# Performance work log

Hardware: AMD Instinct MI355X
Metric: run time of the kernel (lower is better)

Reference implementation:

```python
import jax, jax.numpy as jnp
import numpy as np

N_NODES = 50000
N_EDGES = 800000
F_IN = 128
HID = 32
H_IN = 4
N_CLS = 47
H_OUT = 4
NEG_SLOPE = 0.2


def _param(k, shape, scale=0.1):
    return jax.random.normal(k, shape, dtype=jnp.float32) * scale


def setup_inputs() -> dict:
    key = jax.random.key(0)
    ks = jax.random.split(key, 14)
    return {
        "x": jax.random.normal(ks[0], (N_NODES, F_IN), dtype=jnp.float32),
        "edge_index": jax.random.randint(ks[1], (2, N_EDGES), 0, N_NODES, dtype=jnp.int64),
        # layer 1: in -> hidden, heads_in, concat
        "W1": _param(ks[2], (F_IN, H_IN * HID)),
        "a1s": _param(ks[3], (H_IN, HID)),
        "a1d": _param(ks[4], (H_IN, HID)),
        "b1": _param(ks[5], (H_IN * HID,)),
        # layer 2: hidden*heads -> hidden, heads_in, concat
        "W2": _param(ks[6], (H_IN * HID, H_IN * HID)),
        "a2s": _param(ks[7], (H_IN, HID)),
        "a2d": _param(ks[8], (H_IN, HID)),
        "b2": _param(ks[9], (H_IN * HID,)),
        # layer 3: hidden*heads -> out, heads_out, mean (concat=False)
        "W3": _param(ks[10], (H_IN * HID, H_OUT * N_CLS)),
        "a3s": _param(ks[11], (H_OUT, N_CLS)),
        "a3d": _param(ks[12], (H_OUT, N_CLS)),
        "b3": _param(ks[13], (N_CLS,)),
    }


def gat_conv(x, W, att_src, att_dst, bias, src, dst, concat):
    """PyG GATConv (self-loops pre-appended in src/dst, eval mode)."""
    n = x.shape[0]
    H, C = att_src.shape
    h = (x @ W).reshape(n, H, C)                      # [N, H, C]
    a_src = jnp.sum(h * att_src[None], axis=-1)       # [N, H]
    a_dst = jnp.sum(h * att_dst[None], axis=-1)       # [N, H]
    alpha = a_src[src] + a_dst[dst]                   # [E, H]
    alpha = jnp.where(alpha >= 0, alpha, NEG_SLOPE * alpha)
    # segment softmax over destination nodes
    m = jax.ops.segment_max(alpha, dst, num_segments=n)  # [N, H]
    e = jnp.exp(alpha - m[dst])
    denom = jax.ops.segment_sum(e, dst, num_segments=n)  # [N, H]
    w = e / denom[dst]                                   # [E, H]
    msg = h[src] * w[:, :, None]                         # [E, H, C]
    out = jax.ops.segment_sum(msg, dst, num_segments=n)  # [N, H, C]
    if concat:
        out = out.reshape(n, H * C)
    else:
        out = out.mean(axis=1)
    return out + bias


def reference(x, edge_index, W1, a1s, a1d, b1, W2, a2s, a2d, b2, W3, a3s, a3d, b3):
    n = x.shape[0]
    loops = jnp.arange(n, dtype=edge_index.dtype)
    src = jnp.concatenate([edge_index[0], loops])
    dst = jnp.concatenate([edge_index[1], loops])
    h = gat_conv(x, W1, a1s, a1d, b1, src, dst, concat=True)
    h = jax.nn.relu(h)
    h = gat_conv(h, W2, a2s, a2d, b2, src, dst, concat=True)
    h = jax.nn.relu(h)
    h = gat_conv(h, W3, a3s, a3d, b3, src, dst, concat=False)
    return jax.nn.log_softmax(h, axis=1)
```

## Files before the change

kernel.cpp:

```cpp
#include <hip/hip_runtime.h>

typedef unsigned short u16;
typedef unsigned int uint32;
typedef __attribute__((ext_vector_type(8))) short short8;
typedef __attribute__((ext_vector_type(4))) float float4v;

#define N_NODES 50000
#define N_EDGES 800000
#define N_TOT   850000
#define NBH 256
#define NB_BKT ((N_NODES + 255) >> 8)
#define NODE_BLOCKS ((N_NODES + 3) / 4)

__device__ __forceinline__ float b2f(u16 u) {
  return __uint_as_float(((unsigned int)u) << 16);
}
__device__ __forceinline__ u16 f2b(float f) {
  unsigned int x = __float_as_uint(f);
  unsigned int r = (x + 0x7fffu + ((x >> 16) & 1u)) >> 16;
  return (u16)r;
}
__device__ __forceinline__ float lo_bf(uint32 g) { return __uint_as_float(g << 16); }
__device__ __forceinline__ float hi_bf(uint32 g) { return __uint_as_float(g & 0xffff0000u); }
__device__ __forceinline__ u16 conv_elem(const void* src, int i, int isf32) {
  if (isf32) return f2b(((const float*)src)[i]);
  return ((const u16*)src)[i];
}
__device__ __forceinline__ float lrelu(float a) { return (a >= 0.f) ? a : 0.2f * a; }
__device__ __forceinline__ int eget(const int* __restrict__ ei, int i, int isI64) {
  return isI64 ? ei[2 * i] : ei[i];
}

__global__ void detect_mode(const u16* __restrict__ x16, const int* __restrict__ ei32,
                            int* __restrict__ flags) {
  __shared__ int sh_f32, sh_i32;
  int tid = threadIdx.x;
  if (tid == 0) { sh_f32 = 0; sh_i32 = 0; }
  __syncthreads();
  int emax = 0;
  for (int i = tid; i < 4096; i += 256) {
    int e = (x16[i] >> 7) & 0xFF;
    emax = emax > e ? emax : e;
  }
  if (emax >= 140) atomicOr(&sh_f32, 1);
  if (ei32[2 * tid + 1] != 0) atomicOr(&sh_i32, 1);
  __syncthreads();
  if (tid == 0) { flags[0] = sh_f32; flags[1] = sh_i32 ? 0 : 1; }
}

__global__ void reorder_all(const void* W1, const void* W2, const void* W3,
                            const void* a1s, const void* a1d, const void* b1,
                            const void* a2s, const void* a2d, const void* b2,
                            const void* a3s, const void* a3d, const void* b3,
                            const int* __restrict__ flags,
                            u16* __restrict__ Wf1, u16* __restrict__ Wf2,
                            u16* __restrict__ Wf3, u16* __restrict__ wt) {
  int idx = blockIdx.x * blockDim.x + threadIdx.x;
  int f32 = flags[0];
  if (idx < 57344) {
    const void* W; u16* Wf; int NCOLS, li;
    if (idx < 16384)      { W = W1; Wf = Wf1; NCOLS = 128; li = idx; }
    else if (idx < 32768) { W = W2; Wf = Wf2; NCOLS = 128; li = idx - 16384; }
    else                  { W = W3; Wf = Wf3; NCOLS = 188; li = idx - 32768; }
    int j = li & 7;
    int l = (li >> 3) & 63;
    int c = (li >> 9) & 3;
    int t = li >> 11;
    int k = c * 32 + (l >> 4) * 8 + j;
    int n = t * 16 + (l & 15);
    Wf[li] = (n < NCOLS) ? conv_elem(W, k * NCOLS + n, f32) : (u16)0;
  } else {
    int li = idx - 57344;
    const void* src; int off;
    if (li < 128)       { src = a1s; off = 16384; }
    else if (li < 256)  { src = a1d; off = 16512; li -= 128; }
    else if (li < 384)  { src = b1;  off = 16640; li -= 256; }
    else if (li < 512)  { src = a2s; off = 33152; li -= 384; }
    else if (li < 640)  { src = a2d; off = 33280; li -= 512; }
    else if (li < 768)  { src = b2;  off = 33408; li -= 640; }
    else if (li < 956)  { src = a3s; off = 57600; li -= 768; }
    else if (li < 1144) { src = a3d; off = 57788; li -= 956; }
    else if (li < 1191) { src = b3;  off = 57976; li -= 1144; }
    else return;
    wt[off + li] = conv_elem(src, li, f32);
  }
}


__global__ __launch_bounds__(256) void pack_hist(const int* __restrict__ ei,
                                                 const int* __restrict__ flags,
                                                 uint32* __restrict__ epack,
                                                 int* __restrict__ cnt, int nE) {
  __shared__ int hist[NB_BKT];
  for (int t = threadIdx.x; t < NB_BKT; t += 256) hist[t] = 0;
  __syncthreads();
  const int i64 = flags[1];
  const int chunk = (nE + NBH - 1) / NBH;
  const int lo = blockIdx.x * chunk;
  const int hi = min(lo + chunk, nE);
  for (int e = lo + (int)threadIdx.x; e < hi; e += 256) {
    int s = eget(ei, e, i64);
    int d = eget(ei, nE + e, i64);
    epack[e] = ((uint32)d << 16) | (uint32)s;
    atomicAdd(&hist[d >> 8], 1);
  }
  __syncthreads();
  for (int t = threadIdx.x; t < NB_BKT; t += 256) cnt[t * NBH + blockIdx.x] = hist[t];
}

__global__ __launch_bounds__(256) void scan_cols(int* __restrict__ cnt,
                                                 int* __restrict__ total) {
  __shared__ int ws[4];
  const int bkt = blockIdx.x;
  const int tid = threadIdx.x, lane = tid & 63, wv = tid >> 6;
  int v = cnt[bkt * NBH + tid];
  int incl = v;
#pragma unroll
  for (int off = 1; off < 64; off <<= 1) {
    int t = __shfl_up(incl, off, 64);
    if (lane >= off) incl += t;
  }
  if (lane == 63) ws[wv] = incl;
  __syncthreads();
  if (tid == 0) {
    int s = 0;
#pragma unroll
    for (int w = 0; w < 4; w++) { int t = ws[w]; ws[w] = s; s += t; }
    total[bkt] = s;
  }
  __syncthreads();
  cnt[bkt * NBH + tid] = ws[wv] + incl - v;
}

__global__ __launch_bounds__(256) void scan_base(const int* __restrict__ total,
                                                 int* __restrict__ base) {
  __shared__ int ws[4];
  const int tid = threadIdx.x, lane = tid & 63, wv = tid >> 6;
  int v = (tid < NB_BKT) ? total[tid] : 0;
  int incl = v;
#pragma unroll
  for (int off = 1; off < 64; off <<= 1) {
    int t = __shfl_up(incl, off, 64);
    if (lane >= off) incl += t;
  }
  if (lane == 63) ws[wv] = incl;
  __syncthreads();
  if (tid == 0) {
    int s = 0;
#pragma unroll
    for (int w = 0; w < 4; w++) { int t = ws[w]; ws[w] = s; s += t; }
    base[NB_BKT] = s;
  }
  __syncthreads();
  if (tid < NB_BKT) base[tid] = ws[wv] + incl - v;
}

__global__ __launch_bounds__(256) void scatter_coarse(const uint32* __restrict__ epack,
                                                      const int* __restrict__ cnt,
                                                      const int* __restrict__ base,
                                                      uint32* __restrict__ staging, int nE) {
  __shared__ int lcur[NB_BKT];
  for (int t = threadIdx.x; t < NB_BKT; t += 256)
    lcur[t] = base[t] + cnt[t * NBH + blockIdx.x];
  __syncthreads();
  const int chunk = (nE + NBH - 1) / NBH;
  const int lo = blockIdx.x * chunk;
  const int hi = min(lo + chunk, nE);
  for (int e = lo + (int)threadIdx.x; e < hi; e += 256) {
    uint32 pk = epack[e];
    int p = atomicAdd(&lcur[pk >> 24], 1);
    staging[p] = pk;
  }
}

__global__ __launch_bounds__(256) void build_csr(const uint32* __restrict__ staging,
                                                 const int* __restrict__ base,
                                                 int* __restrict__ row_start,
                                                 int* __restrict__ csr_src32, int nN) {
  __shared__ int hist[256];
  __shared__ int cur[256];
  __shared__ int ws[4];
  const int b = blockIdx.x;
  const int tid = threadIdx.x;
  const int lane = tid & 63, wv = tid >> 6;
  hist[tid] = 0;
  __syncthreads();
  const int lo = base[b], hi = base[b + 1];
  for (int i = lo + tid; i < hi; i += 256)
    atomicAdd(&hist[(staging[i] >> 16) & 255], 1);
  __syncthreads();
  int v = hist[tid];
  int incl = v;
#pragma unroll
  for (int off = 1; off < 64; off <<= 1) {
    int t = __shfl_up(incl, off, 64);
    if (lane >= off) incl += t;
  }
  if (lane == 63) ws[wv] = incl;
  __syncthreads();
  if (tid == 0) {
    int s = 0;
#pragma unroll
    for (int w = 0; w < 4; w++) { int t = ws[w]; ws[w] = s; s += t; }
  }
  __syncthreads();
  int excl = ws[wv] + incl - v;
  const int n = (b << 8) + tid;
  if (n < nN) {
    int rs = lo + (b << 8) + excl + tid;
    row_start[n] = rs;
    csr_src32[rs] = n;
    cur[tid] = rs + 1;
  }
  if (b == NB_BKT - 1 && tid == 0) row_start[nN] = N_TOT;
  __syncthreads();
  for (int i = lo + tid; i < hi; i += 256) {
    uint32 pk = staging[i];
    int p = atomicAdd(&cur[(pk >> 16) & 255], 1);
    csr_src32[p] = (int)(pk & 0xffffu);
  }
}

template <int NT, int NCOLS, int STRIDE, bool FUSE_A, bool CMAJOR, bool FUSE3, bool RAWX>
__global__ __launch_bounds__(256) void gemm_mfma(const void* __restrict__ X,
                                                 const u16* __restrict__ Wf,
                                                 const u16* __restrict__ attS,
                                                 const u16* __restrict__ attD,
                                                 const int* __restrict__ flags,
                                                 u16* __restrict__ H,
                                                 float* __restrict__ a_s,
                                                 float* __restrict__ a_d, int M) {
  const int wid = __builtin_amdgcn_readfirstlane(threadIdx.x >> 6);
  const int lane = threadIdx.x & 63;
  const int row0 = (blockIdx.x * 4 + wid) * 16;
  if (row0 >= M) return;
  const int qr = lane >> 4;
  const int ln = lane & 15;

  float4v acc[NT];
#pragma unroll
  for (int t = 0; t < NT; t++) acc[t] = (float4v){0.f, 0.f, 0.f, 0.f};

  const short8* Wf8 = (const short8*)Wf;
  const size_t aoff = (size_t)(row0 + ln) * 128 + qr * 8;
  int f32m = 0;
  if constexpr (RAWX) f32m = flags[0];

#pragma unroll
  for (int c = 0; c < 4; c++) {
    short8 afrag;
    if constexpr (RAWX) {
      if (f32m) {
        const float* ap = (const float*)X + aoff + c * 32;
        float4 lo = ((const float4*)ap)[0];
        float4 hi = ((const float4*)ap)[1];
        afrag[0] = (short)f2b(lo.x); afrag[1] = (short)f2b(lo.y);
        afrag[2] = (short)f2b(lo.z); afrag[3] = (short)f2b(lo.w);
        afrag[4] = (short)f2b(hi.x); afrag[5] = (short)f2b(hi.y);
        afrag[6] = (short)f2b(hi.z); afrag[7] = (short)f2b(hi.w);
      } else {
        afrag = *(const short8*)((const u16*)X + aoff + c * 32);
      }
    } else {
      afrag = *(const short8*)((const u16*)X + aoff + c * 32);
    }
#pragma unroll
    for (int t = 0; t < NT; t++) {
      short8 bfrag = Wf8[(t * 4 + c) * 64 + lane];
      acc[t] = __builtin_amdgcn_mfma_f32_16x16x32_bf16(afrag, bfrag, acc[t], 0, 0, 0);
    }
  }

#pragma unroll
  for (int t = 0; t < NT; t++) {
    int col = t * 16 + ln;
    if (col < NCOLS) {
      int off;
      if constexpr (CMAJOR) {
        int h = (col >= 141) ? 3 : (col >= 94) ? 2 : (col >= 47) ? 1 : 0;
        int c = col - h * 47;
        off = c * 4 + h;
      } else {
        off = col;
      }
#pragma unroll
      for (int i = 0; i < 4; i++) {
        H[(size_t)(row0 + qr * 4 + i) * STRIDE + off] = f2b(acc[t][i]);
      }
    } else {
      if constexpr (CMAJOR) {
#pragma unroll
        for (int i = 0; i < 4; i++) {
          H[(size_t)(row0 + qr * 4 + i) * STRIDE + col] = (u16)0x3F80;
        }
      }
    }
  }

  if constexpr (FUSE_A) {
    float aSf[NT], aDf[NT];
#pragma unroll
    for (int t = 0; t < NT; t++) {
      aSf[t] = b2f(attS[t * 16 + ln]);
      aDf[t] = b2f(attD[t * 16 + ln]);
    }
#pragma unroll
    for (int h = 0; h < 4; h++) {
#pragma unroll
      for (int i = 0; i < 4; i++) {
        float s = acc[2 * h][i] * aSf[2 * h] + acc[2 * h + 1][i] * aSf[2 * h + 1];
        float d = acc[2 * h][i] * aDf[2 * h] + acc[2 * h + 1][i] * aDf[2 * h + 1];
#pragma unroll
        for (int m = 1; m < 16; m <<= 1) {
          s += __shfl_xor(s, m, 64);
          d += __shfl_xor(d, m, 64);
        }
        if (ln == 0) {
          int r = row0 + qr * 4 + i;
          a_s[r * 4 + h] = s;
          a_d[r * 4 + h] = d;
        }
      }
    }
  }

  if constexpr (FUSE3) {
    float sh[4][4], dh[4][4];
#pragma unroll
    for (int h = 0; h < 4; h++)
#pragma unroll
      for (int i = 0; i < 4; i++) { sh[h][i] = 0.f; dh[h][i] = 0.f; }
#pragma unroll
    for (int t = 0; t < NT; t++) {
      int col = t * 16 + ln;
      bool v = (col < NCOLS);
      float aS = v ? b2f(attS[col]) : 0.f;
      float aD = v ? b2f(attD[col]) : 0.f;
      int hh = (col >= 141) ? 3 : (col >= 94) ? 2 : (col >= 47) ? 1 : 0;
      float aS0 = (hh == 0) ? aS : 0.f, aS1 = (hh == 1) ? aS : 0.f;
      float aS2 = (hh == 2) ? aS : 0.f, aS3 = (hh == 3) ? aS : 0.f;
      float aD0 = (hh == 0) ? aD : 0.f, aD1 = (hh == 1) ? aD : 0.f;
      float aD2 = (hh == 2) ? aD : 0.f, aD3 = (hh == 3) ? aD : 0.f;
#pragma unroll
      for (int i = 0; i < 4; i++) {
        float a = acc[t][i];
        sh[0][i] += a * aS0; sh[1][i] += a * aS1;
        sh[2][i] += a * aS2; sh[3][i] += a * aS3;
        dh[0][i] += a * aD0; dh[1][i] += a * aD1;
        dh[2][i] += a * aD2; dh[3][i] += a * aD3;
      }
    }
#pragma unroll
    for (int h = 0; h < 4; h++) {
#pragma unroll
      for (int i = 0; i < 4; i++) {
        float s = sh[h][i], d = dh[h][i];
#pragma unroll
        for (int m = 1; m < 16; m <<= 1) {
          s += __shfl_xor(s, m, 64);
          d += __shfl_xor(d, m, 64);
        }
        if (ln == 0) {
          int r = row0 + qr * 4 + i;
          a_s[r * 4 + h] = s;
          a_d[r * 4 + h] = d;
        }
      }
    }
  }
}


__global__ __launch_bounds__(256) void aggregate12(const u16* __restrict__ h,
                                                   const float* __restrict__ a_s,
                                                   const float* __restrict__ a_d,
                                                   const int* __restrict__ row_start,
                                                   const int* __restrict__ csr_src,
                                                   const u16* __restrict__ bias,
                                                   u16* __restrict__ out, int nN) {
  const int lane = threadIdx.x & 63;
  const int wid = __builtin_amdgcn_readfirstlane(threadIdx.x >> 6);
  const int n = blockIdx.x * 4 + wid;
  if (n >= nN) return;
  const int hL = lane >> 4;
  const uint32* h32 = (const uint32*)h;
  const float bias0 = b2f(bias[2 * lane]);
  const float bias1 = b2f(bias[2 * lane + 1]);
  const float adv = a_d[n * 4 + hL];
  int beg = row_start[n], end = row_start[n + 1];

  float acc0 = 0.f, acc1 = 0.f, den = 0.f;
  int e = beg;
  for (; e + 3 < end; e += 4) {
    int s[4];
    float av[4];
    uint32 g[4];
#pragma unroll
    for (int j = 0; j < 4; j++) s[j] = csr_src[e + j];
#pragma unroll
    for (int j = 0; j < 4; j++) av[j] = a_s[s[j] * 4 + hL];
#pragma unroll
    for (int j = 0; j < 4; j++) g[j] = h32[s[j] * 64 + lane];
#pragma unroll
    for (int j = 0; j < 4; j++) {
      float w = __expf(lrelu(av[j] + adv));
      den += w;
      acc0 += w * lo_bf(g[j]);
      acc1 += w * hi_bf(g[j]);
    }
  }
  for (; e < end; ++e) {
    int s = csr_src[e];
    float w = __expf(lrelu(a_s[s * 4 + hL] + adv));
    uint32 g = h32[s * 64 + lane];
    den += w;
    acc0 += w * lo_bf(g);
    acc1 += w * hi_bf(g);
  }
  float inv = 1.0f / den;
  float o0 = fmaxf(acc0 * inv + bias0, 0.f);
  float o1 = fmaxf(acc1 * inv + bias1, 0.f);
  uint32 packed = ((uint32)f2b(o1) << 16) | (uint32)f2b(o0);
  ((uint32*)out)[n * 64 + lane] = packed;
}

__global__ __launch_bounds__(256) void aggregate3(const u16* __restrict__ h3,
                                                  const float* __restrict__ a_s,
                                                  const float* __restrict__ a_d,
                                                  const int* __restrict__ row_start,
                                                  const int* __restrict__ csr_src,
                                                  const u16* __restrict__ b3,
                                                  const int* __restrict__ flags,
                                                  void* __restrict__ out, int nN) {
  const int lane = threadIdx.x & 63;
  const int wid = __builtin_amdgcn_readfirstlane(threadIdx.x >> 6);
  const int n = blockIdx.x * 4 + wid;
  if (n >= nN) return;
  const bool act = lane < 47;
  const int lidx = (lane <= 47) ? lane : 0;
  const float b3v = act ? b2f(b3[lane]) : 0.f;
  const int isf32 = flags[0];
  const uint2* h3v = (const uint2*)h3;
  const int wh = (lane - 48) & 3;
  const int lw = (lane >= 48) ? ((lane - 48) >> 2) : 0;
  const float advW = a_d[n * 4 + wh];
  int beg = row_start[n], end = row_start[n + 1];

  float acc0 = 0.f, acc1 = 0.f, acc2 = 0.f, acc3 = 0.f;
  int e = beg;
  for (; e + 7 < end; e += 8) {
    int sA = csr_src[e + lw];
    int sB = csr_src[e + 4 + lw];
    float wA = __expf(lrelu(a_s[sA * 4 + wh] + advW));
    float wB = __expf(lrelu(a_s[sB * 4 + wh] + advW));
    int s[8];
    uint2 g[8];
#pragma unroll
    for (int j = 0; j < 8; j++) s[j] = csr_src[e + j];
#pragma unroll
    for (int j = 0; j < 8; j++) g[j] = h3v[(size_t)s[j] * 48 + lidx];
#pragma unroll
    for (int j = 0; j < 8; j++) {
      const int bl = 48 + (j & 3) * 4;
      float w0, w1, w2, w3;
      if (j < 4) {
        w0 = __shfl(wA, bl + 0, 64); w1 = __shfl(wA, bl + 1, 64);
        w2 = __shfl(wA, bl + 2, 64); w3 = __shfl(wA, bl + 3, 64);
      } else {
        w0 = __shfl(wB, bl + 0, 64); w1 = __shfl(wB, bl + 1, 64);
        w2 = __shfl(wB, bl + 2, 64); w3 = __shfl(wB, bl + 3, 64);
      }
      acc0 += w0 * lo_bf(g[j].x);
      acc1 += w1 * hi_bf(g[j].x);
      acc2 += w2 * lo_bf(g[j].y);
      acc3 += w3 * hi_bf(g[j].y);
    }
  }
  for (; e < end; ++e) {
    int s = csr_src[e];
    float w = __expf(lrelu(a_s[s * 4 + wh] + advW));
    uint2 g = h3v[(size_t)s * 48 + lidx];
    float w0 = __shfl(w, 48, 64);
    float w1 = __shfl(w, 49, 64);
    float w2 = __shfl(w, 50, 64);
    float w3 = __shfl(w, 51, 64);
    acc0 += w0 * lo_bf(g.x);
    acc1 += w1 * hi_bf(g.x);
    acc2 += w2 * lo_bf(g.y);
    acc3 += w3 * hi_bf(g.y);
  }
  float den0 = __shfl(acc0, 47, 64);
  float den1 = __shfl(acc1, 47, 64);
  float den2 = __shfl(acc2, 47, 64);
  float den3 = __shfl(acc3, 47, 64);
  float val = act ? 0.25f * (acc0 / den0 + acc1 / den1 + acc2 / den2 + acc3 / den3) + b3v
                  : -1e30f;
  float mx = val;
#pragma unroll
  for (int m = 1; m < 64; m <<= 1) mx = fmaxf(mx, __shfl_xor(mx, m, 64));
  float ex = act ? __expf(val - mx) : 0.f;
  float sm = ex;
#pragma unroll
  for (int m = 1; m < 64; m <<= 1) sm += __shfl_xor(sm, m, 64);
  float lse = mx + __logf(sm);
  if (act) {
    float r = val - lse;
    if (isf32) ((float*)out)[n * 47 + lane] = r;
    else       ((u16*)out)[n * 47 + lane] = f2b(r);
  }
}


extern "C" void kernel_launch(void* const* d_in, const int* in_sizes, int n_in,
                              void* d_out, int out_size, void* d_ws, size_t ws_size,
                              hipStream_t stream) {
  const void* x   = d_in[0];
  const void* ei  = d_in[1];
  const void* W1  = d_in[2];
  const void* a1s = d_in[3];
  const void* a1d = d_in[4];
  const void* b1  = d_in[5];
  const void* W2  = d_in[6];
  const void* a2s = d_in[7];
  const void* a2d = d_in[8];
  const void* b2  = d_in[9];
  const void* W3  = d_in[10];
  const void* a3s = d_in[11];
  const void* a3d = d_in[12];
  const void* b3  = d_in[13];
  const int* ei32 = (const int*)ei;

  auto au = [](size_t v) { return (v + 255) & ~(size_t)255; };
  char* p = (char*)d_ws;
  int* flags     = (int*)p; p += 256;
  u16* wt        = (u16*)p; p += au((size_t)58023 * 2);
  u16* Wf1       = (u16*)p; p += au((size_t)16384 * 2);
  u16* Wf2       = (u16*)p; p += au((size_t)16384 * 2);
  u16* Wf3       = (u16*)p; p += au((size_t)24576 * 2);
  int* row_start = (int*)p; p += au((size_t)(N_NODES + 1) * 4);
  int* cnt       = (int*)p; p += au((size_t)NB_BKT * NBH * 4);
  int* btotal    = (int*)p; p += au((size_t)NB_BKT * 4);
  int* bbase     = (int*)p; p += au((size_t)(NB_BKT + 1) * 4);
  int* csr_src32 = (int*)p; p += au((size_t)N_TOT * 4);
  float* a_s     = (float*)p; p += au((size_t)N_NODES * 4 * 4);
  float* a_d     = (float*)p; p += au((size_t)N_NODES * 4 * 4);
  u16* hB        = (u16*)p; p += au((size_t)N_NODES * 128 * 2);
  u16* hA        = (u16*)p; p += au((size_t)N_NODES * 128 * 2);
  u16* h3        = (u16*)p; p += au((size_t)N_NODES * 192 * 2);
  uint32* epack   = (uint32*)h3;
  uint32* staging = (uint32*)(h3 + 1600000);

  const u16* a1sc = wt + 16384;
  const u16* a1dc = wt + 16512;
  const u16* b1c  = wt + 16640;
  const u16* a2sc = wt + 33152;
  const u16* a2dc = wt + 33280;
  const u16* b2c  = wt + 33408;
  const u16* a3sc = wt + 57600;
  const u16* a3dc = wt + 57788;
  const u16* b3c  = wt + 57976;

  const int gemmBlocks = (N_NODES / 16 + 3) / 4;

  detect_mode<<<1, 256, 0, stream>>>((const u16*)x, ei32, flags);
  reorder_all<<<229, 256, 0, stream>>>(W1, W2, W3, a1s, a1d, b1, a2s, a2d, b2,
                                       a3s, a3d, b3, flags, Wf1, Wf2, Wf3, wt);

  pack_hist<<<NBH, 256, 0, stream>>>(ei32, flags, epack, cnt, N_EDGES);
  scan_cols<<<NB_BKT, 256, 0, stream>>>(cnt, btotal);
  scan_base<<<1, 256, 0, stream>>>(btotal, bbase);
  scatter_coarse<<<NBH, 256, 0, stream>>>(epack, cnt, bbase, staging, N_EDGES);
  build_csr<<<NB_BKT, 256, 0, stream>>>(staging, bbase, row_start, csr_src32, N_NODES);

  gemm_mfma<8, 128, 128, true, false, false, true><<<gemmBlocks, 256, 0, stream>>>(
      x, Wf1, a1sc, a1dc, flags, hA, a_s, a_d, N_NODES);
  aggregate12<<<NODE_BLOCKS, 256, 0, stream>>>(hA, a_s, a_d, row_start, csr_src32,
                                               b1c, hB, N_NODES);

  gemm_mfma<8, 128, 128, true, false, false, false><<<gemmBlocks, 256, 0, stream>>>(
      hB, Wf2, a2sc, a2dc, flags, hA, a_s, a_d, N_NODES);
  aggregate12<<<NODE_BLOCKS, 256, 0, stream>>>(hA, a_s, a_d, row_start, csr_src32,
                                               b2c, hB, N_NODES);

  gemm_mfma<12, 188, 192, false, true, true, false><<<gemmBlocks, 256, 0, stream>>>(
      hB, Wf3, a3sc, a3dc, flags, h3, a_s, a_d, N_NODES);
  aggregate3<<<NODE_BLOCKS, 256, 0, stream>>>(h3, a_s, a_d, row_start, csr_src32,
                                              b3c, flags, d_out, N_NODES);
}
```

Baseline: 321.5 us.

## Precompute per-edge attention weights for layer 3 in a separate edge kernel

Adds an edge_weights kernel that computes the four per-head exp(leaky_relu) attention weights for every CSR edge and stores them as packed bf16, using a per-edge destination array that build_csr now fills. aggregate3 then loads these weights directly instead of computing exponentials and broadcasting them with lane shuffles, and gains a 4-wide tail loop. This trades shuffle and exp work inside the aggregation for an extra kernel launch, about 8 bytes of weight traffic per edge written and read back, and a serial per-node fill loop in build_csr. Rounding the weights to bf16 also reduces their precision.

```diff
diff --git a/kernel.cpp b/kernel.cpp
--- a/kernel.cpp
+++ b/kernel.cpp
@@ -176,6 +176,7 @@
 __global__ __launch_bounds__(256) void build_csr(const uint32* __restrict__ staging,
                                                  const int* __restrict__ base,
                                                  int* __restrict__ row_start,
+                                                 u16* __restrict__ csr_dst,
                                                  int* __restrict__ csr_src32, int nN) {
   __shared__ int hist[256];
   __shared__ int cur[256];
@@ -210,6 +211,8 @@
     int rs = lo + (b << 8) + excl + tid;
     row_start[n] = rs;
     csr_src32[rs] = n;
+    u16 g16 = (u16)n;
+    for (int k = 0; k <= v; k++) csr_dst[rs + k] = g16;
     cur[tid] = rs + 1;
   }
   if (b == NB_BKT - 1 && tid == 0) row_start[nN] = N_TOT;
@@ -368,6 +371,26 @@
       }
     }
   }
+}
+
+__global__ __launch_bounds__(256) void edge_weights(const int* __restrict__ csr_src,
+                                                    const u16* __restrict__ csr_dst,
+                                                    const float* __restrict__ a_s,
+                                                    const float* __restrict__ a_d,
+                                                    uint2* __restrict__ w, int nE) {
+  int e = blockIdx.x * blockDim.x + threadIdx.x;
+  if (e >= nE) return;
+  int s = csr_src[e], d = csr_dst[e];
+  float4 as = ((const float4*)a_s)[s];
+  float4 ad = ((const float4*)a_d)[d];
+  float w0 = __expf(lrelu(as.x + ad.x));
+  float w1 = __expf(lrelu(as.y + ad.y));
+  float w2 = __expf(lrelu(as.z + ad.z));
+  float w3 = __expf(lrelu(as.w + ad.w));
+  uint2 o;
+  o.x = ((uint32)f2b(w1) << 16) | (uint32)f2b(w0);
+  o.y = ((uint32)f2b(w3) << 16) | (uint32)f2b(w2);
+  w[e] = o;
 }
 
 
@@ -425,8 +448,7 @@
 }
 
 __global__ __launch_bounds__(256) void aggregate3(const u16* __restrict__ h3,
-                                                  const float* __restrict__ a_s,
-                                                  const float* __restrict__ a_d,
+                                                  const uint2* __restrict__ wbuf,
                                                   const int* __restrict__ row_start,
                                                   const int* __restrict__ csr_src,
                                                   const u16* __restrict__ b3,
@@ -441,49 +463,56 @@
   const float b3v = act ? b2f(b3[lane]) : 0.f;
   const int isf32 = flags[0];
   const uint2* h3v = (const uint2*)h3;
-  const int wh = (lane - 48) & 3;
-  const int lw = (lane >= 48) ? ((lane - 48) >> 2) : 0;
-  const float advW = a_d[n * 4 + wh];
   int beg = row_start[n], end = row_start[n + 1];
 
   float acc0 = 0.f, acc1 = 0.f, acc2 = 0.f, acc3 = 0.f;
   int e = beg;
   for (; e + 7 < end; e += 8) {
-    int sA = csr_src[e + lw];
-    int sB = csr_src[e + 4 + lw];
-    float wA = __expf(lrelu(a_s[sA * 4 + wh] + advW));
-    float wB = __expf(lrelu(a_s[sB * 4 + wh] + advW));
     int s[8];
+    uint2 wp[8];
     uint2 g[8];
 #pragma unroll
     for (int j = 0; j < 8; j++) s[j] = csr_src[e + j];
 #pragma unroll
+    for (int j = 0; j < 8; j++) wp[j] = wbuf[e + j];
+#pragma unroll
     for (int j = 0; j < 8; j++) g[j] = h3v[(size_t)s[j] * 48 + lidx];
 #pragma unroll
     for (int j = 0; j < 8; j++) {
-      const int bl = 48 + (j & 3) * 4;
-      float w0, w1, w2, w3;
-      if (j < 4) {
-        w0 = __shfl(wA, bl + 0, 64); w1 = __shfl(wA, bl + 1, 64);
-        w2 = __shfl(wA, bl + 2, 64); w3 = __shfl(wA, bl + 3, 64);
-      } else {
-        w0 = __shfl(wB, bl + 0, 64); w1 = __shfl(wB, bl + 1, 64);
-        w2 = __shfl(wB, bl + 2, 64); w3 = __shfl(wB, bl + 3, 64);
-      }
+      float w0 = lo_bf(wp[j].x), w1 = hi_bf(wp[j].x);
+      float w2 = lo_bf(wp[j].y), w3 = hi_bf(wp[j].y);
       acc0 += w0 * lo_bf(g[j].x);
       acc1 += w1 * hi_bf(g[j].x);
       acc2 += w2 * lo_bf(g[j].y);
       acc3 += w3 * hi_bf(g[j].y);
     }
   }
+  for (; e + 3 < end; e += 4) {
+    int s[4];
+    uint2 wp[4];
+    uint2 g[4];
+#pragma unroll
+    for (int j = 0; j < 4; j++) s[j] = csr_src[e + j];
+#pragma unroll
+    for (int j = 0; j < 4; j++) wp[j] = wbuf[e + j];
+#pragma unroll
+    for (int j = 0; j < 4; j++) g[j] = h3v[(size_t)s[j] * 48 + lidx];
+#pragma unroll
+    for (int j = 0; j < 4; j++) {
+      float w0 = lo_bf(wp[j].x), w1 = hi_bf(wp[j].x);
+      float w2 = lo_bf(wp[j].y), w3 = hi_bf(wp[j].y);
+      acc0 += w0 * lo_bf(g[j].x);
+      acc1 += w1 * hi_bf(g[j].x);
+      acc2 += w2 * lo_bf(g[j].y);
+      acc3 += w3 * hi_bf(g[j].y);
+    }
+  }
   for (; e < end; ++e) {
     int s = csr_src[e];
-    float w = __expf(lrelu(a_s[s * 4 + wh] + advW));
+    uint2 wp = wbuf[e];
     uint2 g = h3v[(size_t)s * 48 + lidx];
-    float w0 = __shfl(w, 48, 64);
-    float w1 = __shfl(w, 49, 64);
-    float w2 = __shfl(w, 50, 64);
-    float w3 = __shfl(w, 51, 64);
+    float w0 = lo_bf(wp.x), w1 = hi_bf(wp.x);
+    float w2 = lo_bf(wp.y), w3 = hi_bf(wp.y);
     acc0 += w0 * lo_bf(g.x);
     acc1 += w1 * hi_bf(g.x);
     acc2 += w2 * lo_bf(g.y);
@@ -542,6 +571,8 @@
   int* btotal    = (int*)p; p += au((size_t)NB_BKT * 4);
   int* bbase     = (int*)p; p += au((size_t)(NB_BKT + 1) * 4);
   int* csr_src32 = (int*)p; p += au((size_t)N_TOT * 4);
+  u16* csr_dst   = (u16*)p; p += au((size_t)N_TOT * 2);
+  uint2* wbuf    = (uint2*)p; p += au((size_t)N_TOT * 8);
   float* a_s     = (float*)p; p += au((size_t)N_NODES * 4 * 4);
   float* a_d     = (float*)p; p += au((size_t)N_NODES * 4 * 4);
   u16* hB        = (u16*)p; p += au((size_t)N_NODES * 128 * 2);
@@ -561,6 +592,7 @@
   const u16* b3c  = wt + 57976;
 
   const int gemmBlocks = (N_NODES / 16 + 3) / 4;
+  const int edgeBlocks = (N_TOT + 255) / 256;
 
   detect_mode<<<1, 256, 0, stream>>>((const u16*)x, ei32, flags);
   reorder_all<<<229, 256, 0, stream>>>(W1, W2, W3, a1s, a1d, b1, a2s, a2d, b2,
@@ -570,7 +602,8 @@
   scan_cols<<<NB_BKT, 256, 0, stream>>>(cnt, btotal);
   scan_base<<<1, 256, 0, stream>>>(btotal, bbase);
   scatter_coarse<<<NBH, 256, 0, stream>>>(epack, cnt, bbase, staging, N_EDGES);
-  build_csr<<<NB_BKT, 256, 0, stream>>>(staging, bbase, row_start, csr_src32, N_NODES);
+  build_csr<<<NB_BKT, 256, 0, stream>>>(staging, bbase, row_start, csr_dst,
+                                        csr_src32, N_NODES);
 
   gemm_mfma<8, 128, 128, true, false, false, true><<<gemmBlocks, 256, 0, stream>>>(
       x, Wf1, a1sc, a1dc, flags, hA, a_s, a_d, N_NODES);
@@ -584,6 +617,7 @@
 
   gemm_mfma<12, 188, 192, false, true, true, false><<<gemmBlocks, 256, 0, stream>>>(
       hB, Wf3, a3sc, a3dc, flags, h3, a_s, a_d, N_NODES);
-  aggregate3<<<NODE_BLOCKS, 256, 0, stream>>>(h3, a_s, a_d, row_start, csr_src32,
+  edge_weights<<<edgeBlocks, 256, 0, stream>>>(csr_src32, csr_dst, a_s, a_d, wbuf, N_TOT);
+  aggregate3<<<NODE_BLOCKS, 256, 0, stream>>>(h3, wbuf, row_start, csr_src32,
                                               b3c, flags, d_out, N_NODES);
 }
```

Measured after the change: 311.7 us. 3.0% less time.
